# Optimization experiments

Measured on AMD Instinct MI355X. Metric: run time of the kernel, lower is better.

## Reference

```python
import jax, jax.numpy as jnp
import numpy as np

EPS = 1e-8  # torch F.cosine_similarity default eps


def setup_inputs() -> dict:
    key = jax.random.key(0)
    k1, k2 = jax.random.split(key)
    x = jax.random.normal(k1, (16384, 512), dtype=jnp.float32)
    weights = jax.random.normal(k2, (4096, 512), dtype=jnp.float32)
    return {"x": x, "weights": weights}


def _l2_normalize(v):
    # matches torch cosine_similarity: divide by max(||v||, eps)
    norm = jnp.sqrt(jnp.sum(v * v, axis=-1, keepdims=True))
    return v / jnp.maximum(norm, EPS)


def reference(x, weights):
    # nested-loop cosine similarity == normalized GEMM
    xn = _l2_normalize(x)        # [B, D]
    wn = _l2_normalize(weights)  # [N, D]
    return jnp.einsum('bd,nd->bn', xn, wn)  # [B, N]
```

## Files before the change

kernel.cpp:

```cpp
#include <hip/hip_runtime.h>
#include <hip/hip_bf16.h>

typedef __attribute__((ext_vector_type(8))) short bf16x8;
typedef __attribute__((ext_vector_type(4))) float f32x4;

#define DIM 512
#define BM 128
#define BN 128
#define BK 32

static __device__ __forceinline__ unsigned short f2bf_rne(float f) {
    unsigned int u = __float_as_uint(f);
    u += 0x7fffu + ((u >> 16) & 1u);
    return (unsigned short)(u >> 16);
}

static __device__ __forceinline__ void async16(const void* g, void* l) {
    __builtin_amdgcn_global_load_lds((const __attribute__((address_space(1))) unsigned int*)g,
                                     (__attribute__((address_space(3))) unsigned int*)l,
                                     16, 0, 0);
}

__global__ __launch_bounds__(256) void norm_rows_kernel(const float* __restrict__ src,
                                                        unsigned short* __restrict__ dst,
                                                        int nrows) {
    int gw   = (blockIdx.x * 256 + threadIdx.x) >> 6;
    int lane = threadIdx.x & 63;
    if (gw >= nrows) return;
    const float4* row = reinterpret_cast<const float4*>(src + (size_t)gw * DIM);
    float4 v0 = row[2 * lane];
    float4 v1 = row[2 * lane + 1];
    float ss = v0.x*v0.x + v0.y*v0.y + v0.z*v0.z + v0.w*v0.w
             + v1.x*v1.x + v1.y*v1.y + v1.z*v1.z + v1.w*v1.w;
    #pragma unroll
    for (int off = 32; off >= 1; off >>= 1) ss += __shfl_xor(ss, off);
    float scale = 1.0f / fmaxf(sqrtf(ss), 1e-8f);
    bf16x8 o;
    o[0] = (short)f2bf_rne(v0.x * scale);
    o[1] = (short)f2bf_rne(v0.y * scale);
    o[2] = (short)f2bf_rne(v0.z * scale);
    o[3] = (short)f2bf_rne(v0.w * scale);
    o[4] = (short)f2bf_rne(v1.x * scale);
    o[5] = (short)f2bf_rne(v1.y * scale);
    o[6] = (short)f2bf_rne(v1.z * scale);
    o[7] = (short)f2bf_rne(v1.w * scale);
    *reinterpret_cast<bf16x8*>(dst + (size_t)gw * DIM + lane * 8) = o;
}

__global__ __launch_bounds__(256) void cos_gemm_kernel(const unsigned short* __restrict__ A,
                                                       const unsigned short* __restrict__ Bm,
                                                       float* __restrict__ C,
                                                       int M, int N, int K) {
    __shared__ __align__(16) unsigned short As[BM * BK];
    __shared__ __align__(16) unsigned short Bs[BN * BK];

    int nwg = gridDim.x;
    int bid = blockIdx.x;
    int cpx = nwg >> 3;
    int swz = (bid & 7) * cpx + (bid >> 3);
    int nbn = N / BN;
    int bm = swz / nbn;
    int bn = swz % nbn;

    int tid  = threadIdx.x;
    int lane = tid & 63;
    int wv   = tid >> 6;
    int wr   = wv >> 1;
    int wc   = wv & 1;
    int fr   = lane & 15;
    int kq   = lane >> 4;

    int boff0 = tid * 16;
    int boff1 = boff0 + 4096;
    int row0 = boff0 >> 6, ce0 = (boff0 & 63) >> 1;
    int row1 = boff1 >> 6, ce1 = (boff1 & 63) >> 1;

    const unsigned short* aSrc0 = A  + (size_t)(bm * BM + row0) * K + ce0;
    const unsigned short* aSrc1 = A  + (size_t)(bm * BM + row1) * K + ce1;
    const unsigned short* bSrc0 = Bm + (size_t)(bn * BN + row0) * K + ce0;
    const unsigned short* bSrc1 = Bm + (size_t)(bn * BN + row1) * K + ce1;

    f32x4 acc[4][4] = {};

    const int kTiles = K / BK;
    for (int kt = 0; kt < kTiles; ++kt) {
        int ko = kt * BK;
        async16(aSrc0 + ko, (char*)As + boff0);
        async16(aSrc1 + ko, (char*)As + boff1);
        async16(bSrc0 + ko, (char*)Bs + boff0);
        async16(bSrc1 + ko, (char*)Bs + boff1);
        __syncthreads();

        bf16x8 af[4], bfr[4];
        #pragma unroll
        for (int m = 0; m < 4; ++m)
            af[m] = *reinterpret_cast<const bf16x8*>(
                (const char*)As + (wr * 64 + m * 16 + fr) * 64 + kq * 16);
        #pragma unroll
        for (int n = 0; n < 4; ++n)
            bfr[n] = *reinterpret_cast<const bf16x8*>(
                (const char*)Bs + (wc * 64 + n * 16 + fr) * 64 + kq * 16);

        #pragma unroll
        for (int m = 0; m < 4; ++m)
            #pragma unroll
            for (int n = 0; n < 4; ++n)
                acc[m][n] = __builtin_amdgcn_mfma_f32_16x16x32_bf16(
                    af[m], bfr[n], acc[m][n], 0, 0, 0);
        __syncthreads();
    }

    float* Cblk = C + (size_t)(bm * BM + wr * 64) * N + bn * BN + wc * 64;
    #pragma unroll
    for (int m = 0; m < 4; ++m)
        #pragma unroll
        for (int n = 0; n < 4; ++n)
            #pragma unroll
            for (int j = 0; j < 4; ++j)
                Cblk[(size_t)(m * 16 + kq * 4 + j) * N + n * 16 + fr] = acc[m][n][j];
}

extern "C" void kernel_launch(void* const* d_in, const int* in_sizes, int n_in,
                              void* d_out, int out_size, void* d_ws, size_t ws_size,
                              hipStream_t stream) {
    const float* x = (const float*)d_in[0];
    const float* w = (const float*)d_in[1];
    float* out = (float*)d_out;
    int B = in_sizes[0] / DIM;
    int N = in_sizes[1] / DIM;

    unsigned short* xn = (unsigned short*)d_ws;
    unsigned short* wn = xn + (size_t)B * DIM;

    norm_rows_kernel<<<(B + 3) / 4, 256, 0, stream>>>(x, xn, B);
    norm_rows_kernel<<<(N + 3) / 4, 256, 0, stream>>>(w, wn, N);

    int grid = (B / BM) * (N / BN);
    cos_gemm_kernel<<<grid, 256, 0, stream>>>(xn, wn, out, B, N, DIM);
}
```

Baseline: 371.4 us.

## Enlarge GEMM tiles, double-buffer LDS with prefetch, and swizzle LDS layout

```diff
diff --git a/kernel.cpp b/kernel.cpp
--- a/kernel.cpp
+++ b/kernel.cpp
@@ -5,9 +5,10 @@
 typedef __attribute__((ext_vector_type(4))) float f32x4;
 
 #define DIM 512
-#define BM 128
-#define BN 128
-#define BK 32
+#define BM 256
+#define BN 256
+#define BK 64
+#define NKT (DIM / BK)
 
 static __device__ __forceinline__ unsigned short f2bf_rne(float f) {
     unsigned int u = __float_as_uint(f);
@@ -47,12 +48,13 @@
     *reinterpret_cast<bf16x8*>(dst + (size_t)gw * DIM + lane * 8) = o;
 }
 
-__global__ __launch_bounds__(256) void cos_gemm_kernel(const unsigned short* __restrict__ A,
-                                                       const unsigned short* __restrict__ Bm,
-                                                       float* __restrict__ C,
-                                                       int M, int N, int K) {
-    __shared__ __align__(16) unsigned short As[BM * BK];
-    __shared__ __align__(16) unsigned short Bs[BN * BK];
+__global__ __launch_bounds__(512, 2) void cos_gemm_kernel(const unsigned short* __restrict__ A,
+                                                          const unsigned short* __restrict__ Bm,
+                                                          float* __restrict__ C) {
+    __shared__ __align__(16) unsigned short lds[2][2][BM * BK];
+
+    const int M = 16384, N = 4096, K = 512;
+    (void)M;
 
     int nwg = gridDim.x;
     int bid = blockIdx.x;
@@ -65,59 +67,85 @@
     int tid  = threadIdx.x;
     int lane = tid & 63;
     int wv   = tid >> 6;
-    int wr   = wv >> 1;
-    int wc   = wv & 1;
+    int wr   = wv >> 2;
+    int wc   = wv & 3;
     int fr   = lane & 15;
     int kq   = lane >> 4;
 
-    int boff0 = tid * 16;
-    int boff1 = boff0 + 4096;
-    int row0 = boff0 >> 6, ce0 = (boff0 & 63) >> 1;
-    int row1 = boff1 >> 6, ce1 = (boff1 & 63) >> 1;
+    int srow[4], scol[4];
+    #pragma unroll
+    for (int i = 0; i < 4; ++i) {
+        int s = tid + 512 * i;
+        int r = s >> 3;
+        int c = (s & 7) ^ (r & 7);
+        srow[i] = r;
+        scol[i] = c * 8;
+    }
+    const unsigned short* Abase = A  + (size_t)(bm * BM) * K;
+    const unsigned short* Bbase = Bm + (size_t)(bn * BN) * K;
 
-    const unsigned short* aSrc0 = A  + (size_t)(bm * BM + row0) * K + ce0;
-    const unsigned short* aSrc1 = A  + (size_t)(bm * BM + row1) * K + ce1;
-    const unsigned short* bSrc0 = Bm + (size_t)(bn * BN + row0) * K + ce0;
-    const unsigned short* bSrc1 = Bm + (size_t)(bn * BN + row1) * K + ce1;
+    f32x4 acc[8][4] = {};
 
-    f32x4 acc[4][4] = {};
+    #pragma unroll
+    for (int i = 0; i < 4; ++i) {
+        async16(Abase + (size_t)srow[i] * K + scol[i],
+                (char*)&lds[0][0][0] + (tid + 512 * i) * 16);
+        async16(Bbase + (size_t)srow[i] * K + scol[i],
+                (char*)&lds[0][1][0] + (tid + 512 * i) * 16);
+    }
+    __syncthreads();
 
-    const int kTiles = K / BK;
-    for (int kt = 0; kt < kTiles; ++kt) {
-        int ko = kt * BK;
-        async16(aSrc0 + ko, (char*)As + boff0);
-        async16(aSrc1 + ko, (char*)As + boff1);
-        async16(bSrc0 + ko, (char*)Bs + boff0);
-        async16(bSrc1 + ko, (char*)Bs + boff1);
+    int cur = 0;
+    for (int kt = 0; kt < NKT; ++kt) {
+        if (kt + 1 < NKT) {
+            int nxt = cur ^ 1;
+            int ko = (kt + 1) * BK;
+            #pragma unroll
+            for (int i = 0; i < 4; ++i) {
+                async16(Abase + (size_t)srow[i] * K + ko + scol[i],
+                        (char*)&lds[nxt][0][0] + (tid + 512 * i) * 16);
+                async16(Bbase + (size_t)srow[i] * K + ko + scol[i],
+                        (char*)&lds[nxt][1][0] + (tid + 512 * i) * 16);
+            }
+        }
+        const char* Abuf = (const char*)&lds[cur][0][0];
+        const char* Bbuf = (const char*)&lds[cur][1][0];
+        #pragma unroll
+        for (int kk = 0; kk < 2; ++kk) {
+            int q = kk * 4 + kq;
+            bf16x8 af[8], bfv[4];
+            #pragma unroll
+            for (int m = 0; m < 8; ++m) {
+                int row  = wr * 128 + m * 16 + fr;
+                int slot = row * 8 + (q ^ (row & 7));
+                af[m] = *reinterpret_cast<const bf16x8*>(Abuf + slot * 16);
+            }
+            #pragma unroll
+            for (int n = 0; n < 4; ++n) {
+                int row  = wc * 64 + n * 16 + fr;
+                int slot = row * 8 + (q ^ (row & 7));
+                bfv[n] = *reinterpret_cast<const bf16x8*>(Bbuf + slot * 16);
+            }
+            #pragma unroll
+            for (int m = 0; m < 8; ++m)
+                #pragma unroll
+                for (int n = 0; n < 4; ++n)
+                    acc[m][n] = __builtin_amdgcn_mfma_f32_16x16x32_bf16(
+                        af[m], bfv[n], acc[m][n], 0, 0, 0);
+        }
         __syncthreads();
-
-        bf16x8 af[4], bfr[4];
-        #pragma unroll
-        for (int m = 0; m < 4; ++m)
-            af[m] = *reinterpret_cast<const bf16x8*>(
-                (const char*)As + (wr * 64 + m * 16 + fr) * 64 + kq * 16);
-        #pragma unroll
-        for (int n = 0; n < 4; ++n)
-            bfr[n] = *reinterpret_cast<const bf16x8*>(
-                (const char*)Bs + (wc * 64 + n * 16 + fr) * 64 + kq * 16);
-
-        #pragma unroll
-        for (int m = 0; m < 4; ++m)
-            #pragma unroll
-            for (int n = 0; n < 4; ++n)
-                acc[m][n] = __builtin_amdgcn_mfma_f32_16x16x32_bf16(
-                    af[m], bfr[n], acc[m][n], 0, 0, 0);
-        __syncthreads();
+        cur ^= 1;
     }
 
-    float* Cblk = C + (size_t)(bm * BM + wr * 64) * N + bn * BN + wc * 64;
+    size_t crow0 = (size_t)(bm * BM + wr * 128);
+    int    ccol0 = bn * BN + wc * 64;
     #pragma unroll
-    for (int m = 0; m < 4; ++m)
+    for (int m = 0; m < 8; ++m)
         #pragma unroll
         for (int n = 0; n < 4; ++n)
             #pragma unroll
             for (int j = 0; j < 4; ++j)
-                Cblk[(size_t)(m * 16 + kq * 4 + j) * N + n * 16 + fr] = acc[m][n][j];
+                C[(crow0 + m * 16 + kq * 4 + j) * N + ccol0 + n * 16 + fr] = acc[m][n][j];
 }
 
 extern "C" void kernel_launch(void* const* d_in, const int* in_sizes, int n_in,
@@ -136,5 +164,5 @@
     norm_rows_kernel<<<(N + 3) / 4, 256, 0, stream>>>(w, wn, N);
 
     int grid = (B / BM) * (N / BN);
-    cos_gemm_kernel<<<grid, 256, 0, stream>>>(xn, wn, out, B, N, DIM);
+    cos_gemm_kernel<<<grid, 512, 0, stream>>>(xn, wn, out);
 }
```

After: 343.5 us. 7.5% less time.
